# Kernel optimization log

Measured on AMD Instinct MI355X. Metric: run time of the kernel, lower is better.

## Reference

```python
import jax, jax.numpy as jnp
import numpy as np

N, F, D, H = 8192, 128, 128, 2
LEAKY_ALPHA = 0.3  # keras.layers.LeakyReLU default


def setup_inputs() -> dict:
    key = jax.random.key(0)
    ks = jax.random.split(key, 8)
    x = jax.random.normal(ks[0], (N, F), dtype=jnp.float32)
    # sparse-ish binary adjacency with self loops, stored dense (as the module does)
    adj = (jax.random.uniform(ks[1], (N, N)) < 0.01).astype(jnp.float32)
    adj = jnp.clip(adj + jnp.eye(N, dtype=jnp.float32), 0.0, 1.0)
    s = 1.0 / np.sqrt(F)
    Wmap = jax.random.normal(ks[2], (H, F, D), dtype=jnp.float32) * s
    a1_w = jax.random.normal(ks[3], (H, D), dtype=jnp.float32) * (1.0 / np.sqrt(D))
    a2_w = jax.random.normal(ks[4], (H, D), dtype=jnp.float32) * (1.0 / np.sqrt(D))
    a1_b = jnp.zeros((H,), dtype=jnp.float32)
    a2_b = jnp.zeros((H,), dtype=jnp.float32)
    kernel = jax.random.normal(ks[5], (H, F, D), dtype=jnp.float32) * s
    bias = jnp.zeros((H, N, D), dtype=jnp.float32)
    return {"x": x, "adj": adj, "Wmap": Wmap, "a1_w": a1_w, "a1_b": a1_b,
            "a2_w": a2_w, "a2_b": a2_b, "kernel": kernel, "bias": bias}


def reference(x, adj, Wmap, a1_w, a1_b, a2_w, a2_b, kernel, bias):
    # per-head Conv1D(k=1, no bias): node-wise linear map  [H, N, D]
    mapped = jnp.einsum('nf,hfd->hnd', x, Wmap)
    # per-head Conv1D(k=1) scalar scores  [H, N]
    sa1 = jnp.einsum('hnd,hd->hn', mapped, a1_w) + a1_b[:, None]
    sa2 = jnp.einsum('hnd,hd->hn', mapped, a2_w) + a2_b[:, None]
    # additive score masked multiplicatively by adjacency:  [H, N, N]
    w = adj[None, :, :] * sa1[:, :, None] + adj[None, :, :] * sa2[:, None, :]
    w = jnp.where(w >= 0, w, LEAKY_ALPHA * w)
    att = jax.nn.softmax(w, axis=-1)  # softmax over neighbors (incl. zeroed entries, as in source)
    value = jnp.einsum('nf,hfd->hnd', x, kernel)
    out = jnp.einsum('hnm,hmd->hnd', att, value) + bias  # [H, N, D]
    return out.mean(axis=0)  # attn_heads_reduction='average', linear activation
```

## Files before the change

### kernel.cpp

```cpp
#include <hip/hip_runtime.h>
#include <hip/hip_bf16.h>

#define NN 8192
#define FF 128
#define DD 128
#define HH 2
#define ALPHA 0.3f
#define MAXNNZ 1024

typedef float vfloat4 __attribute__((ext_vector_type(4)));

__global__ __launch_bounds__(256) void prep_kernel(
    const float* __restrict__ x, const float* __restrict__ kern,
    const float* __restrict__ Wmap, const float* __restrict__ a1w,
    const float* __restrict__ a2w, const float* __restrict__ a1b,
    const float* __restrict__ a2b, unsigned short* __restrict__ value_bf,
    float* __restrict__ colsum, float* __restrict__ sa1, float* __restrict__ sa2) {
  int h = blockIdx.y;
  int row0 = blockIdx.x * 32;
  __shared__ float Bl[64 * 128];
  __shared__ float Al[32 * 129];
  __shared__ float cvec[2][128];
  const float4* Bg4 = (const float4*)(kern + (size_t)h * FF * DD);
  const float4* Ag4 = (const float4*)(x + (size_t)row0 * FF);
  float4* Bl4 = (float4*)Bl;
  int tid = threadIdx.x;

  #pragma unroll
  for (int q = 0; q < 4; q++) {
    int idx = q * 256 + tid;
    int r = idx >> 5, c4 = idx & 31;
    float4 g = Ag4[idx];
    Al[r * 129 + c4 * 4 + 0] = g.x;
    Al[r * 129 + c4 * 4 + 1] = g.y;
    Al[r * 129 + c4 * 4 + 2] = g.z;
    Al[r * 129 + c4 * 4 + 3] = g.w;
  }

  {
    int which = tid >> 7, f = tid & 127;
    const float4* w4 = (const float4*)(Wmap + ((size_t)h * FF + f) * DD);
    const float4* av4 = (const float4*)((which ? a2w : a1w) + (size_t)h * DD);
    float s = 0.f;
    #pragma unroll 8
    for (int dq = 0; dq < 32; dq++) {
      float4 w = w4[dq];
      float4 a = av4[dq];
      s += w.x * a.x + w.y * a.y + w.z * a.z + w.w * a.w;
    }
    cvec[which][f] = s;
  }
  __syncthreads();

  if (tid < 64) {
    int r = tid & 31, type = tid >> 5;
    const float* cv = cvec[type];
    float s = 0.f;
    #pragma unroll 8
    for (int f = 0; f < 128; f++) s += Al[r * 129 + f] * cv[f];
    float b = type ? a2b[h] : a1b[h];
    float* dst = type ? sa2 : sa1;
    dst[(size_t)h * NN + row0 + r] = s + b;
  }

  int cg = tid & 31;
  int rg = tid >> 5;
  float4 acc[4];
  #pragma unroll
  for (int m = 0; m < 4; m++) acc[m] = make_float4(0.f, 0.f, 0.f, 0.f);

  for (int kp = 0; kp < 2; kp++) {
    __syncthreads();
    #pragma unroll
    for (int q = 0; q < 8; q++)
      Bl4[q * 256 + tid] = Bg4[kp * 2048 + q * 256 + tid];
    __syncthreads();
    for (int k2 = 0; k2 < 64; k2++) {
      int k = kp * 64 + k2;
      float4 bv = *(const float4*)&Bl[k2 * 128 + cg * 4];
      #pragma unroll
      for (int m = 0; m < 4; m++) {
        float av = Al[(rg + m * 8) * 129 + k];
        acc[m].x += av * bv.x;
        acc[m].y += av * bv.y;
        acc[m].z += av * bv.z;
        acc[m].w += av * bv.w;
      }
    }
  }

  #pragma unroll
  for (int m = 0; m < 4; m++) {
    int r = row0 + rg + m * 8;
    ushort4 pk;
    __hip_bfloat16 b0 = __float2bfloat16(acc[m].x);
    __hip_bfloat16 b1 = __float2bfloat16(acc[m].y);
    __hip_bfloat16 b2 = __float2bfloat16(acc[m].z);
    __hip_bfloat16 b3 = __float2bfloat16(acc[m].w);
    pk.x = *(unsigned short*)&b0;
    pk.y = *(unsigned short*)&b1;
    pk.z = *(unsigned short*)&b2;
    pk.w = *(unsigned short*)&b3;
    *(ushort4*)&value_bf[((size_t)h * NN + r) * DD + cg * 4] = pk;
  }

  float4 cp;
  cp.x = acc[0].x + acc[1].x + acc[2].x + acc[3].x;
  cp.y = acc[0].y + acc[1].y + acc[2].y + acc[3].y;
  cp.z = acc[0].z + acc[1].z + acc[2].z + acc[3].z;
  cp.w = acc[0].w + acc[1].w + acc[2].w + acc[3].w;
  __syncthreads();
  float* colred = Al;
  *(float4*)&colred[rg * 128 + cg * 4] = cp;
  __syncthreads();
  if (rg == 0) {
    #pragma unroll
    for (int c = 0; c < 4; c++) {
      int col = cg * 4 + c;
      float s = 0.f;
      #pragma unroll
      for (int rr = 0; rr < 8; rr++) s += colred[rr * 128 + col];
      atomicAdd(&colsum[h * DD + col], s);
    }
  }
}

__global__ __launch_bounds__(256) void gat_main(
    const float* __restrict__ adj, const float* __restrict__ sa1,
    const float* __restrict__ sa2, const unsigned short* __restrict__ value_bf,
    const float* __restrict__ colsum, const float* __restrict__ bias,
    float* __restrict__ out) {
  int i = blockIdx.x;
  __shared__ int idxbuf[MAXNNZ];
  __shared__ float em1buf[HH][MAXNNZ];
  __shared__ int cnt;
  __shared__ float sume_sh[HH];
  __shared__ float wred[4][HH];
  __shared__ float contrib[256];
  int t = threadIdx.x;
  int lane = t & 63;
  if (t == 0) cnt = 0;
  __syncthreads();

  const vfloat4* arow = (const vfloat4*)(adj + (size_t)i * NN);
  #pragma unroll
  for (int q = 0; q < 8; q++) {
    int f4 = q * 256 + t;
    vfloat4 a = __builtin_nontemporal_load(&arow[f4]);
    int j0 = f4 * 4;
    #pragma unroll
    for (int c = 0; c < 4; c++) {
      bool nz = (a[c] != 0.f);
      unsigned long long m = __ballot(nz);
      int tot = __popcll(m);
      int base = 0;
      if (lane == 0 && tot) base = atomicAdd(&cnt, tot);
      base = __shfl(base, 0);
      if (nz) {
        int p = base + __popcll(m & ((1ull << lane) - 1ull));
        if (p < MAXNNZ) idxbuf[p] = j0 + c;
      }
    }
  }
  __syncthreads();
  int count = min(cnt, MAXNNZ);

  float s10 = sa1[i];
  float s11 = sa1[NN + i];
  float l0 = 0.f, l1 = 0.f;
  for (int k = t; k < count; k += 256) {
    int j = idxbuf[k];
    float w0 = s10 + sa2[j];
    float w1 = s11 + sa2[NN + j];
    w0 = (w0 >= 0.f) ? w0 : ALPHA * w0;
    w1 = (w1 >= 0.f) ? w1 : ALPHA * w1;
    float e0 = __expf(w0) - 1.f;
    float e1 = __expf(w1) - 1.f;
    em1buf[0][k] = e0;
    em1buf[1][k] = e1;
    l0 += e0;
    l1 += e1;
  }
  #pragma unroll
  for (int o = 32; o > 0; o >>= 1) {
    l0 += __shfl_down(l0, o);
    l1 += __shfl_down(l1, o);
  }
  int wid = t >> 6;
  if (lane == 0) { wred[wid][0] = l0; wred[wid][1] = l1; }
  __syncthreads();
  if (t == 0) {
    sume_sh[0] = wred[0][0] + wred[1][0] + wred[2][0] + wred[3][0];
    sume_sh[1] = wred[0][1] + wred[1][1] + wred[2][1] + wred[3][1];
  }
  __syncthreads();

  int h = t >> 7, d = t & 127;
  const unsigned short* val = value_bf + (size_t)h * NN * DD + d;
  const float* eb = em1buf[h];
  float acc = 0.f;
  #pragma unroll 4
  for (int k = 0; k < count; k++) {
    int j = idxbuf[k];
    unsigned short u = val[(size_t)j * DD];
    __hip_bfloat16 bv = *(__hip_bfloat16*)&u;
    acc += eb[k] * __bfloat162float(bv);
  }
  float denom = (float)NN + sume_sh[h];
  float bb = __builtin_nontemporal_load(&bias[((size_t)h * NN + i) * DD + d]);
  float r = (colsum[h * DD + d] + acc) / denom + bb;
  contrib[t] = r;
  __syncthreads();
  if (t < 64) {
    float2 o2;
    o2.x = 0.5f * (contrib[2 * t]     + contrib[2 * t + 128]);
    o2.y = 0.5f * (contrib[2 * t + 1] + contrib[2 * t + 129]);
    *(float2*)&out[(size_t)i * DD + 2 * t] = o2;
  }
}

extern "C" void kernel_launch(void* const* d_in, const int* in_sizes, int n_in,
                              void* d_out, int out_size, void* d_ws, size_t ws_size,
                              hipStream_t stream) {
  const float* x    = (const float*)d_in[0];
  const float* adj  = (const float*)d_in[1];
  const float* Wmap = (const float*)d_in[2];
  const float* a1w  = (const float*)d_in[3];
  const float* a1b  = (const float*)d_in[4];
  const float* a2w  = (const float*)d_in[5];
  const float* a2b  = (const float*)d_in[6];
  const float* kern = (const float*)d_in[7];
  const float* bias = (const float*)d_in[8];
  float* out = (float*)d_out;
  float* ws  = (float*)d_ws;

  float* sa1    = ws;
  float* sa2    = ws + 16384;
  float* colsum = ws + 32768;
  unsigned short* value_bf = (unsigned short*)(ws + 33024);

  (void)hipMemsetAsync(colsum, 0, HH * DD * sizeof(float), stream);
  prep_kernel<<<dim3(NN / 32, HH), 256, 0, stream>>>(
      x, kern, Wmap, a1w, a2w, a1b, a2b, value_bf, colsum, sa1, sa2);
  gat_main<<<NN, 256, 0, stream>>>(adj, sa1, sa2, value_bf, colsum, bias, out);
}
```

Before: 460.6 us.

## Batch adjacency loads, per-thread atomic compaction, and split neighbor gather across wave halves

The adjacency row loads are all issued up front. Compaction now does one shared-atomic per thread with a 4-wide nonzero count, replacing the per-element ballot/shuffle sequence. The value gather is reorganised so each wave handles one head and half of the neighbor list, with each lane reading two packed bf16 values. Partial sums are then combined through shared memory. This aims to raise memory-level parallelism and cut instruction count, but neighbor order in idxbuf becomes nondeterministic and shared-atomic contention rises.

```diff
diff --git a/kernel.cpp b/kernel.cpp
--- a/kernel.cpp
+++ b/kernel.cpp
@@ -136,29 +136,31 @@
   __shared__ int cnt;
   __shared__ float sume_sh[HH];
   __shared__ float wred[4][HH];
-  __shared__ float contrib[256];
+  __shared__ float red[4][128];
   int t = threadIdx.x;
   int lane = t & 63;
+  int wave = t >> 6;
   if (t == 0) cnt = 0;
   __syncthreads();
 
   const vfloat4* arow = (const vfloat4*)(adj + (size_t)i * NN);
+  vfloat4 av[8];
+  #pragma unroll
+  for (int q = 0; q < 8; q++)
+    av[q] = __builtin_nontemporal_load(&arow[q * 256 + t]);
   #pragma unroll
   for (int q = 0; q < 8; q++) {
-    int f4 = q * 256 + t;
-    vfloat4 a = __builtin_nontemporal_load(&arow[f4]);
-    int j0 = f4 * 4;
-    #pragma unroll
-    for (int c = 0; c < 4; c++) {
-      bool nz = (a[c] != 0.f);
-      unsigned long long m = __ballot(nz);
-      int tot = __popcll(m);
-      int base = 0;
-      if (lane == 0 && tot) base = atomicAdd(&cnt, tot);
-      base = __shfl(base, 0);
-      if (nz) {
-        int p = base + __popcll(m & ((1ull << lane) - 1ull));
-        if (p < MAXNNZ) idxbuf[p] = j0 + c;
+    vfloat4 a = av[q];
+    int nz4 = (a[0] != 0.f) + (a[1] != 0.f) + (a[2] != 0.f) + (a[3] != 0.f);
+    if (nz4) {
+      int p = atomicAdd(&cnt, nz4);
+      int j0 = (q * 256 + t) * 4;
+      #pragma unroll
+      for (int c = 0; c < 4; c++) {
+        if (a[c] != 0.f) {
+          if (p < MAXNNZ) idxbuf[p] = j0 + c;
+          p++;
+        }
       }
     }
   }
@@ -186,36 +188,45 @@
     l0 += __shfl_down(l0, o);
     l1 += __shfl_down(l1, o);
   }
-  int wid = t >> 6;
-  if (lane == 0) { wred[wid][0] = l0; wred[wid][1] = l1; }
+  if (lane == 0) { wred[wave][0] = l0; wred[wave][1] = l1; }
   __syncthreads();
   if (t == 0) {
     sume_sh[0] = wred[0][0] + wred[1][0] + wred[2][0] + wred[3][0];
     sume_sh[1] = wred[0][1] + wred[1][1] + wred[2][1] + wred[3][1];
   }
-  __syncthreads();
-
-  int h = t >> 7, d = t & 127;
-  const unsigned short* val = value_bf + (size_t)h * NN * DD + d;
+
+  int h = wave >> 1;
+  int half = wave & 1;
+  int d0 = lane * 2;
+  const unsigned short* val = value_bf + (size_t)h * NN * DD + d0;
   const float* eb = em1buf[h];
-  float acc = 0.f;
-  #pragma unroll 4
-  for (int k = 0; k < count; k++) {
+  float ax = 0.f, ay = 0.f;
+  for (int k = half; k < count; k += 2) {
     int j = idxbuf[k];
-    unsigned short u = val[(size_t)j * DD];
-    __hip_bfloat16 bv = *(__hip_bfloat16*)&u;
-    acc += eb[k] * __bfloat162float(bv);
-  }
-  float denom = (float)NN + sume_sh[h];
-  float bb = __builtin_nontemporal_load(&bias[((size_t)h * NN + i) * DD + d]);
-  float r = (colsum[h * DD + d] + acc) / denom + bb;
-  contrib[t] = r;
-  __syncthreads();
-  if (t < 64) {
-    float2 o2;
-    o2.x = 0.5f * (contrib[2 * t]     + contrib[2 * t + 128]);
-    o2.y = 0.5f * (contrib[2 * t + 1] + contrib[2 * t + 129]);
-    *(float2*)&out[(size_t)i * DD + 2 * t] = o2;
+    unsigned int u = *(const unsigned int*)&val[(size_t)j * DD];
+    float e = eb[k];
+    unsigned short ulo = (unsigned short)(u & 0xffff);
+    unsigned short uhi = (unsigned short)(u >> 16);
+    __hip_bfloat16 blo = *(__hip_bfloat16*)&ulo;
+    __hip_bfloat16 bhi = *(__hip_bfloat16*)&uhi;
+    ax += e * __bfloat162float(blo);
+    ay += e * __bfloat162float(bhi);
+  }
+  red[wave][d0] = ax;
+  red[wave][d0 + 1] = ay;
+  __syncthreads();
+
+  if (t < 128) {
+    int d = t;
+    float acc0 = red[0][d] + red[1][d];
+    float acc1 = red[2][d] + red[3][d];
+    float denom0 = (float)NN + sume_sh[0];
+    float denom1 = (float)NN + sume_sh[1];
+    float b0 = bias[(size_t)i * DD + d];
+    float b1 = bias[(size_t)NN * DD + (size_t)i * DD + d];
+    float r0 = (colsum[d] + acc0) / denom0 + b0;
+    float r1 = (colsum[DD + d] + acc1) / denom1 + b1;
+    out[(size_t)i * DD + d] = 0.5f * (r0 + r1);
   }
 }
 
```

After: 462.8 us. No clear change (+0.5%).
